# Kernel tuning notes

Hardware: AMD Instinct MI355X
Metric: run time of the kernel (lower is better)

## Reference

```python
import jax, jax.numpy as jnp
import numpy as np

N = 50000   # nodes
E = 800000  # edges
G = 64      # graphs in batch
EPS = 1e-5  # BatchNorm eps


def setup_inputs() -> dict:
    key = jax.random.key(0)
    ks = jax.random.split(key, 32)
    inp = {
        'x': jax.random.normal(ks[0], (N, 1), jnp.float32),
        'edge_index': jax.random.randint(ks[1], (2, E), 0, N),
        'batch': jnp.sort(jax.random.randint(ks[2], (N,), 0, G)),
    }
    dims = [(1, 64), (64, 64), (64, 64), (64, 64)]
    for i, (din, dout) in enumerate(dims, 1):
        inp[f'W{i}'] = jax.random.normal(ks[2 + i], (din, dout), jnp.float32) / np.sqrt(din)
        inp[f'b{i}'] = jnp.zeros((dout,), jnp.float32)
        inp[f'g{i}'] = jnp.ones((dout,), jnp.float32)
        inp[f'bt{i}'] = jnp.zeros((dout,), jnp.float32)
    inp['fw1'] = jax.random.normal(ks[10], (128, 64), jnp.float32) / 8.0
    inp['fb1'] = jnp.zeros((128,), jnp.float32)
    inp['fw2'] = jax.random.normal(ks[11], (10, 128), jnp.float32) / np.sqrt(128)
    inp['fb2'] = jnp.zeros((10,), jnp.float32)
    return inp


def _gcn_norm(edge_index):
    # add self-loops, symmetric normalization (PyG GCNConv default)
    loop = jnp.arange(N)
    row = jnp.concatenate([edge_index[0], loop])
    col = jnp.concatenate([edge_index[1], loop])
    deg = jax.ops.segment_sum(jnp.ones_like(col, jnp.float32), col, num_segments=N)
    dinv = jnp.where(deg > 0, deg ** -0.5, 0.0)
    norm = dinv[row] * dinv[col]
    return row, col, norm


def _gcn(x, W, b, row, col, norm):
    h = x @ W                                   # [N, dout]
    msg = h[row] * norm[:, None]                # gather + scale per edge
    agg = jax.ops.segment_sum(msg, col, num_segments=N)  # scatter-add
    return agg + b


def _bn(x, g, bt):
    m = x.mean(0)
    v = x.var(0)
    return g * (x - m) * jax.lax.rsqrt(v + EPS) + bt


def reference(x, edge_index, batch,
              W1, b1, g1, bt1, W2, b2, g2, bt2,
              W3, b3, g3, bt3, W4, b4, g4, bt4,
              fw1, fb1, fw2, fb2):
    row, col, norm = _gcn_norm(edge_index)
    x = jax.nn.relu(_bn(_gcn(x, W1, b1, row, col, norm), g1, bt1))
    x = jax.nn.relu(_bn(_gcn(x, W2, b2, row, col, norm), g2, bt2))
    x = jax.nn.relu(_bn(_gcn(x, W3, b3, row, col, norm), g3, bt3))
    x = jax.nn.relu(_bn(_gcn(x, W4, b4, row, col, norm), g4, bt4))
    # global mean pool over graphs
    cnt = jax.ops.segment_sum(jnp.ones((N,), jnp.float32), batch, num_segments=G)
    pooled = jax.ops.segment_sum(x, batch, num_segments=G) / jnp.clip(cnt, 1.0)[:, None]
    h = jax.nn.relu(pooled @ fw1.T + fb1)
    return h @ fw2.T + fb2
```

## Files before the change

kernel.cpp:

```cpp
#include <hip/hip_runtime.h>

#define NN 50000
#define NE 800000
#define NG 64
#define FD 64
#define BN_EPS 1e-5f
#define SCAN_B 256
#define NBIN 98
#define BINCAP 12288
#define SCH 4096
#define SCH_NBLK ((NE + SCH - 1) / SCH)
#define INV_NN (1.0f / NN)

__global__ __launch_bounds__(256) void k_binscatter(const int* __restrict__ row,
                                                    const int* __restrict__ col,
                                                    int* __restrict__ gcnt,
                                                    int* __restrict__ bins) {
    __shared__ int stage[SCH];
    __shared__ int cnt[NBIN], off[NBIN + 1], cur[NBIN], gbase[NBIN];
    int t = threadIdx.x;
    int e0 = blockIdx.x * SCH;
    int nk = NE - e0; if (nk > SCH) nk = SCH;
    if (nk <= 0) return;
    for (int b = t; b < NBIN; b += 256) cnt[b] = 0;
    __syncthreads();
    for (int k = t; k < nk; k += 256) {
        int c = col[e0 + k];
        atomicAdd(&cnt[c >> 9], 1);
    }
    __syncthreads();
    if (t == 0) {
        int run = 0;
        for (int b = 0; b < NBIN; ++b) { off[b] = run; run += cnt[b]; }
        off[NBIN] = run;
    }
    __syncthreads();
    if (t < NBIN) {
        cur[t] = off[t];
        gbase[t] = t * BINCAP + atomicAdd(&gcnt[t], cnt[t]);
    }
    __syncthreads();
    for (int k = t; k < nk; k += 256) {
        int c = col[e0 + k];
        int r = row[e0 + k];
        int b = c >> 9;
        int pos = atomicAdd(&cur[b], 1);
        stage[pos] = ((c & 511) << 16) | r;
    }
    __syncthreads();
    for (int k = t; k < nk; k += 256) {
        int lo = 0, hi = NBIN - 1;
        while (lo < hi) {
            int mid = (lo + hi + 1) >> 1;
            if (off[mid] <= k) lo = mid; else hi = mid - 1;
        }
        bins[gbase[lo] + (k - off[lo])] = stage[k];
    }
}

__global__ __launch_bounds__(256) void k_binscan(const int* __restrict__ gcnt,
                                                 const int* __restrict__ bins,
                                                 const float* __restrict__ x,
                                                 int* __restrict__ cursor,
                                                 int* __restrict__ bsum,
                                                 float* __restrict__ dinv,
                                                 float* __restrict__ xd) {
    __shared__ int ldeg[512];
    __shared__ int psc[256];
    int b = blockIdx.x, t = threadIdx.x;
    for (int l = t; l < 512; l += 256) ldeg[l] = 0;
    __syncthreads();
    int nb = gcnt[b];
    const int* bp = bins + b * BINCAP;
    for (int k = t; k < nb; k += 256) atomicAdd(&ldeg[bp[k] >> 16], 1);
    __syncthreads();
    int d0 = ldeg[2 * t], d1 = ldeg[2 * t + 1];
    int pv = d0 + d1;
    psc[t] = pv;
    __syncthreads();
    for (int off = 1; off < 256; off <<= 1) {
        int u = (t >= off) ? psc[t - off] : 0;
        __syncthreads();
        psc[t] += u;
        __syncthreads();
    }
    int excl = psc[t] - pv;
    int base = b << 9;
    int i0 = base + 2 * t, i1 = i0 + 1;
    if (i0 < NN) {
        cursor[i0] = excl;
        float dv = rsqrtf((float)d0 + 1.0f);
        dinv[i0] = dv; xd[i0] = x[i0] * dv;
    }
    if (i1 < NN) {
        cursor[i1] = excl + d0;
        float dv = rsqrtf((float)d1 + 1.0f);
        dinv[i1] = dv; xd[i1] = x[i1] * dv;
    }
    if (t == 255) bsum[b] = psc[255];
}

__global__ __launch_bounds__(SCAN_B) void k_scan_top(int* __restrict__ bsum,
                                                     float* __restrict__ stats) {
    __shared__ int sh[SCAN_B];
    int t = threadIdx.x;
    if (t < 2) stats[t] = 0.0f;
    int v = (t < NBIN) ? bsum[t] : 0;
    sh[t] = v;
    __syncthreads();
    for (int off = 1; off < SCAN_B; off <<= 1) {
        int u = (t >= off) ? sh[t - off] : 0;
        __syncthreads();
        sh[t] += u;
        __syncthreads();
    }
    if (t < NBIN) bsum[t] = sh[t] - v;
}

__global__ __launch_bounds__(256) void k_binfill(const int* __restrict__ gcnt,
                                                 const int* __restrict__ bins,
                                                 const int* __restrict__ cursor,
                                                 const int* __restrict__ bsum,
                                                 int* __restrict__ eidx) {
    __shared__ int lcur[512];
    int b = blockIdx.x, t = threadIdx.x;
    int base = b << 9;
    int bofs = bsum[b];
    for (int l = t; l < 512; l += 256) {
        int i = base + l;
        lcur[l] = (i < NN) ? cursor[i] + bofs : 0;
    }
    __syncthreads();
    int nb = gcnt[b];
    const int* bp = bins + b * BINCAP;
    for (int k = t; k < nb; k += 256) {
        int v = bp[k];
        int pos = atomicAdd(&lcur[v >> 16], 1);
        eidx[pos] = v & 0xFFFF;
    }
}

__global__ __launch_bounds__(256) void k_l1_gather(const int* __restrict__ cursor,
                                                   const int* __restrict__ bsum,
                                                   const int* __restrict__ eidx,
                                                   const float* __restrict__ xd,
                                                   const float* __restrict__ x,
                                                   const float* __restrict__ dinv,
                                                   float* __restrict__ s,
                                                   float* __restrict__ stats) {
    __shared__ float ls[256], lq[256];
    int t = threadIdx.x;
    int i = blockIdx.x * 256 + t;
    float sv = 0.0f;
    if (i < NN) {
        int start = cursor[i] + bsum[i >> 9];
        int end = (i < NN - 1) ? cursor[i + 1] + bsum[(i + 1) >> 9] : NE;
        float acc = 0.0f;
        for (int k = start; k < end; ++k) acc += xd[eidx[k]];
        float di = dinv[i];
        sv = di * (acc + di * x[i]);
        s[i] = sv;
    }
    ls[t] = sv; lq[t] = sv * sv;
    __syncthreads();
    for (int st = 128; st > 0; st >>= 1) {
        if (t < st) { ls[t] += ls[t + st]; lq[t] += lq[t + st]; }
        __syncthreads();
    }
    if (t == 0) { atomicAdd(&stats[0], ls[0]); atomicAdd(&stats[1], lq[0]); }
}

__global__ __launch_bounds__(256) void k_mm_l1(const float* __restrict__ s,
                                               const float* __restrict__ stats,
                                               const float* __restrict__ W1,
                                               const float* __restrict__ g1,
                                               const float* __restrict__ bt1,
                                               const float* __restrict__ W,
                                               float* __restrict__ h) {
    __shared__ float Ws[64 * 64];
    __shared__ float xs[4 * 64];
    __shared__ float als[64], cls[64];
    int t = threadIdx.x;
    for (int k = t; k < 64 * 64; k += 256) Ws[k] = W[k];
    if (t < 64) {
        float mean = stats[0] * INV_NN;
        float var  = stats[1] * INV_NN - mean * mean;
        float w = W1[t];
        float rinv = rsqrtf(var * w * w + BN_EPS);
        float a = g1[t] * w * rinv;
        als[t] = a;
        cls[t] = bt1[t] - a * mean;
    }
    __syncthreads();
    int n0 = blockIdx.x * 4;
    int j = t & 63, n = t >> 6;
    int node = n0 + n;
    float sv = (node < NN) ? s[node] : 0.0f;
    xs[t] = fmaxf(als[j] * sv + cls[j], 0.0f);
    __syncthreads();
    if (node < NN) {
        float acc = 0.f;
        #pragma unroll
        for (int k = 0; k < 64; ++k) acc += xs[n * 64 + k] * Ws[k * 64 + j];
        h[node * 64 + j] = acc;
    }
}

__global__ __launch_bounds__(256) void k_mm_bn(const float* __restrict__ src,
                                               const float* __restrict__ bnsum,
                                               const float* __restrict__ bnsq,
                                               const float* __restrict__ g,
                                               const float* __restrict__ bt,
                                               const float* __restrict__ W,
                                               float* __restrict__ h) {
    __shared__ float Ws[64 * 64];
    __shared__ float xs[4 * 64];
    __shared__ float scl[64], shf[64];
    int t = threadIdx.x;
    for (int k = t; k < 64 * 64; k += 256) Ws[k] = W[k];
    if (t < 64) {
        float mean = bnsum[t] * INV_NN;
        float var  = bnsq[t] * INV_NN - mean * mean;
        float rinv = rsqrtf(var + BN_EPS);
        float sc = g[t] * rinv;
        scl[t] = sc;
        shf[t] = bt[t] - sc * mean;
    }
    __syncthreads();
    int n0 = blockIdx.x * 4;
    int j = t & 63, n = t >> 6;
    int node = n0 + n;
    int gidx = n0 * 64 + t;
    float v = (gidx < NN * 64) ? src[gidx] : 0.0f;
    xs[t] = fmaxf(scl[j] * v + shf[j], 0.0f);
    __syncthreads();
    if (node < NN) {
        float acc = 0.f;
        #pragma unroll
        for (int k = 0; k < 64; ++k) acc += xs[n * 64 + k] * Ws[k * 64 + j];
        h[node * 64 + j] = acc;
    }
}

__global__ __launch_bounds__(256) void k_gather(const int* __restrict__ cursor,
                                                const int* __restrict__ bsum,
                                                const int* __restrict__ eidx,
                                                const float* __restrict__ dinv,
                                                const float* __restrict__ h,
                                                const float* __restrict__ b,
                                                float* __restrict__ agg,
                                                float* __restrict__ bnsumz,
                                                float* __restrict__ bnsqz) {
    if (blockIdx.x == 0) {
        int t = threadIdx.x;
        if (t < 64) bnsumz[t] = 0.0f;
        else if (t < 128) bnsqz[t - 64] = 0.0f;
    }
    int node = blockIdx.x * 4 + (threadIdx.x >> 6);
    if (node >= NN) return;
    int lane = threadIdx.x & 63;
    int eslot = lane >> 4;
    int fb = (lane & 15) << 2;
    int start = cursor[node] + bsum[node >> 9];
    int end = (node < NN - 1) ? cursor[node + 1] + bsum[(node + 1) >> 9] : NE;
    float4 acc = make_float4(0.f, 0.f, 0.f, 0.f);
    for (int e = start + eslot; e < end; e += 4) {
        int r = eidx[e];
        float dr = dinv[r];
        const float4 hv = *reinterpret_cast<const float4*>(&h[r * 64 + fb]);
        acc.x += hv.x * dr; acc.y += hv.y * dr; acc.z += hv.z * dr; acc.w += hv.w * dr;
    }
    acc.x += __shfl_xor(acc.x, 16); acc.y += __shfl_xor(acc.y, 16);
    acc.z += __shfl_xor(acc.z, 16); acc.w += __shfl_xor(acc.w, 16);
    acc.x += __shfl_xor(acc.x, 32); acc.y += __shfl_xor(acc.y, 32);
    acc.z += __shfl_xor(acc.z, 32); acc.w += __shfl_xor(acc.w, 32);
    if (lane < 16) {
        float dc = dinv[node];
        const float4 hv = *reinterpret_cast<const float4*>(&h[node * 64 + fb]);
        const float4 bv = *reinterpret_cast<const float4*>(&b[fb]);
        float4 o;
        o.x = dc * (acc.x + dc * hv.x) + bv.x;
        o.y = dc * (acc.y + dc * hv.y) + bv.y;
        o.z = dc * (acc.z + dc * hv.z) + bv.z;
        o.w = dc * (acc.w + dc * hv.w) + bv.w;
        *reinterpret_cast<float4*>(&agg[node * 64 + fb]) = o;
    }
}

__global__ __launch_bounds__(256) void k_bn_stats(const float* __restrict__ agg,
                                                  float* __restrict__ bnsum, float* __restrict__ bnsq,
                                                  float* __restrict__ pooledz, float* __restrict__ cntz) {
    if (pooledz != nullptr && blockIdx.x == 0) {
        for (int k = threadIdx.x; k < 64 * 64; k += 256) pooledz[k] = 0.0f;
        if (threadIdx.x < 64) cntz[threadIdx.x] = 0.0f;
    }
    __shared__ float ls[256], lq[256];
    int j = threadIdx.x & 63, nl = threadIdx.x >> 6;
    float a = 0.f, b = 0.f;
    for (int i = blockIdx.x * 4 + nl; i < NN; i += gridDim.x * 4) {
        float v = agg[i * 64 + j]; a += v; b += v * v;
    }
    ls[threadIdx.x] = a; lq[threadIdx.x] = b; __syncthreads();
    if (threadIdx.x < 128) { ls[threadIdx.x] += ls[threadIdx.x + 128]; lq[threadIdx.x] += lq[threadIdx.x + 128]; }
    __syncthreads();
    if (threadIdx.x < 64) {
        atomicAdd(&bnsum[j], ls[threadIdx.x] + ls[threadIdx.x + 64]);
        atomicAdd(&bnsq[j],  lq[threadIdx.x] + lq[threadIdx.x + 64]);
    }
}

__global__ __launch_bounds__(256) void k_pool_bn(const float* __restrict__ agg,
                                                 const float* __restrict__ bnsum,
                                                 const float* __restrict__ bnsq,
                                                 const float* __restrict__ g4,
                                                 const float* __restrict__ bt4,
                                                 const int* __restrict__ batch,
                                                 float* __restrict__ pooled,
                                                 float* __restrict__ cnt) {
    const int wpb = 4;
    int wave = blockIdx.x * wpb + (threadIdx.x >> 6);
    int lane = threadIdx.x & 63;
    const int nwaves = gridDim.x * wpb;
    int chunk = (NN + nwaves - 1) / nwaves;
    int i0 = wave * chunk;
    int i1 = i0 + chunk; if (i1 > NN) i1 = NN;
    if (i0 >= NN) return;
    float mean = bnsum[lane] * INV_NN;
    float var  = bnsq[lane] * INV_NN - mean * mean;
    float rinv = rsqrtf(var + BN_EPS);
    float sc = g4[lane] * rinv;
    float sh = bt4[lane] - sc * mean;
    float acc = 0.0f;
    int curb = batch[i0];
    int runlen = 0;
    for (int i = i0; i < i1; ++i) {
        int b = batch[i];
        if (b != curb) {
            atomicAdd(&pooled[curb * 64 + lane], acc);
            if (lane == 0) atomicAdd(&cnt[curb], (float)runlen);
            acc = 0.0f; runlen = 0; curb = b;
        }
        acc += fmaxf(sc * agg[i * 64 + lane] + sh, 0.0f);
        ++runlen;
    }
    atomicAdd(&pooled[curb * 64 + lane], acc);
    if (lane == 0) atomicAdd(&cnt[curb], (float)runlen);
}

__global__ __launch_bounds__(128) void k_fc(const float* __restrict__ pooled, const float* __restrict__ cnt,
                                            const float* __restrict__ fw1, const float* __restrict__ fb1,
                                            const float* __restrict__ fw2, const float* __restrict__ fb2,
                                            float* __restrict__ out) {
    __shared__ float p[64], hsh[128];
    int g = blockIdx.x, t = threadIdx.x;
    if (t < 64) {
        float c = cnt[g]; c = c < 1.f ? 1.f : c;
        p[t] = pooled[g * 64 + t] / c;
    }
    __syncthreads();
    float acc = fb1[t];
    #pragma unroll 8
    for (int k = 0; k < 64; ++k) acc += p[k] * fw1[t * 64 + k];
    hsh[t] = fmaxf(acc, 0.f);
    __syncthreads();
    if (t < 10) {
        float o = fb2[t];
        #pragma unroll 8
        for (int k = 0; k < 128; ++k) o += hsh[k] * fw2[t * 128 + k];
        out[g * 10 + t] = o;
    }
}

extern "C" void kernel_launch(void* const* d_in, const int* in_sizes, int n_in,
                              void* d_out, int out_size, void* d_ws, size_t ws_size,
                              hipStream_t stream) {
    const float* x   = (const float*)d_in[0];
    const int* ei    = (const int*)d_in[1];
    const int* batch = (const int*)d_in[2];
    const float* W[5]  = {nullptr, (const float*)d_in[3],  (const float*)d_in[7],
                                   (const float*)d_in[11], (const float*)d_in[15]};
    const float* bb[5] = {nullptr, (const float*)d_in[4],  (const float*)d_in[8],
                                   (const float*)d_in[12], (const float*)d_in[16]};
    const float* gg[5] = {nullptr, (const float*)d_in[5],  (const float*)d_in[9],
                                   (const float*)d_in[13], (const float*)d_in[17]};
    const float* bt[5] = {nullptr, (const float*)d_in[6],  (const float*)d_in[10],
                                   (const float*)d_in[14], (const float*)d_in[18]};
    const float* fw1 = (const float*)d_in[19];
    const float* fb1 = (const float*)d_in[20];
    const float* fw2 = (const float*)d_in[21];
    const float* fb2 = (const float*)d_in[22];
    float* out = (float*)d_out;

    const int* row = ei;
    const int* col = ei + NE;

    float* ws = (float*)d_ws;
    int*   cursor  = (int*)ws;
    int*   eidx    = (int*)(ws + 50000);
    float* dinv    = ws + 850000;
    float* xd      = ws + 900000;
    int*   bsum    = (int*)(ws + 950000);
    float* s       = ws + 951000;
    float* stats   = ws + 1001008;
    float* bnsum   = ws + 1001072;
    float* bnsq    = ws + 1001136;
    float* pooled  = ws + 1001360;
    float* cnt     = ws + 1005456;
    int*   gcnt    = (int*)(ws + 1056000);
    float* hbuf    = ws + 1100000;
    int*   bins    = (int*)(ws + 1100000);
    float* aggbuf  = ws + 4300000;

    const int B = 256;
    int gN = (NN + B - 1) / B;

    hipMemsetAsync(gcnt, 0, NBIN * sizeof(int), stream);
    k_binscatter<<<SCH_NBLK, B, 0, stream>>>(row, col, gcnt, bins);
    k_binscan<<<NBIN, B, 0, stream>>>(gcnt, bins, x, cursor, bsum, dinv, xd);
    k_scan_top<<<1, SCAN_B, 0, stream>>>(bsum, stats);
    k_binfill<<<NBIN, B, 0, stream>>>(gcnt, bins, cursor, bsum, eidx);

    k_l1_gather<<<gN, B, 0, stream>>>(cursor, bsum, eidx, xd, x, dinv, s, stats);

    k_mm_l1<<<(NN + 3) / 4, B, 0, stream>>>(s, stats, W[1], gg[1], bt[1], W[2], hbuf);
    k_gather<<<(NN + 3) / 4, B, 0, stream>>>(cursor, bsum, eidx, dinv, hbuf, bb[2], aggbuf, bnsum, bnsq);
    k_bn_stats<<<512, B, 0, stream>>>(aggbuf, bnsum, bnsq, nullptr, nullptr);

    for (int L = 3; L <= 4; ++L) {
        k_mm_bn<<<(NN + 3) / 4, B, 0, stream>>>(aggbuf, bnsum, bnsq, gg[L - 1], bt[L - 1], W[L], hbuf);
        k_gather<<<(NN + 3) / 4, B, 0, stream>>>(cursor, bsum, eidx, dinv, hbuf, bb[L], aggbuf, bnsum, bnsq);
        k_bn_stats<<<512, B, 0, stream>>>(aggbuf, bnsum, bnsq,
                                          (L == 4) ? pooled : nullptr, (L == 4) ? cnt : nullptr);
    }

    k_pool_bn<<<512, B, 0, stream>>>(aggbuf, bnsum, bnsq, gg[4], bt[4], batch, pooled, cnt);
    k_fc<<<NG, 128, 0, stream>>>(pooled, cnt, fw1, fb1, fw2, fb2, out);
}
```

Baseline: 345.7 us.

## Fuse BN statistics into gather epilogue and merge binfill with layer-1 gather

```diff
diff --git a/kernel.cpp b/kernel.cpp
--- a/kernel.cpp
+++ b/kernel.cpp
@@ -11,6 +11,8 @@
 #define SCH 4096
 #define SCH_NBLK ((NE + SCH - 1) / SCH)
 #define INV_NN (1.0f / NN)
+#define NSLOT 256
+#define MM_NBLK ((NN + 3) / 4)
 
 __global__ __launch_bounds__(256) void k_binscatter(const int* __restrict__ row,
                                                     const int* __restrict__ col,
@@ -117,18 +119,25 @@
     if (t < NBIN) bsum[t] = sh[t] - v;
 }
 
-__global__ __launch_bounds__(256) void k_binfill(const int* __restrict__ gcnt,
-                                                 const int* __restrict__ bins,
-                                                 const int* __restrict__ cursor,
-                                                 const int* __restrict__ bsum,
-                                                 int* __restrict__ eidx) {
-    __shared__ int lcur[512];
+__global__ __launch_bounds__(256) void k_binfill_l1(const int* __restrict__ gcnt,
+                                                    const int* __restrict__ bins,
+                                                    const int* __restrict__ cursor,
+                                                    const int* __restrict__ bsum,
+                                                    int* __restrict__ eidx,
+                                                    const float* __restrict__ xd,
+                                                    const float* __restrict__ x,
+                                                    const float* __restrict__ dinv,
+                                                    float* __restrict__ s,
+                                                    float* __restrict__ stats) {
+    __shared__ int lstart[512], lcur[512];
+    __shared__ float ls[256], lq[256];
     int b = blockIdx.x, t = threadIdx.x;
     int base = b << 9;
     int bofs = bsum[b];
     for (int l = t; l < 512; l += 256) {
         int i = base + l;
-        lcur[l] = (i < NN) ? cursor[i] + bofs : 0;
+        int st = (i < NN) ? cursor[i] + bofs : 0;
+        lstart[l] = st; lcur[l] = st;
     }
     __syncthreads();
     int nb = gcnt[b];
@@ -138,30 +147,23 @@
         int pos = atomicAdd(&lcur[v >> 16], 1);
         eidx[pos] = v & 0xFFFF;
     }
-}
-
-__global__ __launch_bounds__(256) void k_l1_gather(const int* __restrict__ cursor,
-                                                   const int* __restrict__ bsum,
-                                                   const int* __restrict__ eidx,
-                                                   const float* __restrict__ xd,
-                                                   const float* __restrict__ x,
-                                                   const float* __restrict__ dinv,
-                                                   float* __restrict__ s,
-                                                   float* __restrict__ stats) {
-    __shared__ float ls[256], lq[256];
-    int t = threadIdx.x;
-    int i = blockIdx.x * 256 + t;
-    float sv = 0.0f;
-    if (i < NN) {
-        int start = cursor[i] + bsum[i >> 9];
-        int end = (i < NN - 1) ? cursor[i + 1] + bsum[(i + 1) >> 9] : NE;
-        float acc = 0.0f;
-        for (int k = start; k < end; ++k) acc += xd[eidx[k]];
-        float di = dinv[i];
-        sv = di * (acc + di * x[i]);
-        s[i] = sv;
-    }
-    ls[t] = sv; lq[t] = sv * sv;
+    __syncthreads();
+    float a = 0.0f, q = 0.0f;
+    #pragma unroll
+    for (int half = 0; half < 2; ++half) {
+        int l = t + half * 256;
+        int i = base + l;
+        if (i < NN) {
+            float acc = 0.0f;
+            int e0 = lstart[l], e1 = lcur[l];
+            for (int k = e0; k < e1; ++k) acc += xd[eidx[k]];
+            float di = dinv[i];
+            float sv = di * (acc + di * x[i]);
+            s[i] = sv;
+            a += sv; q += sv * sv;
+        }
+    }
+    ls[t] = a; lq[t] = q;
     __syncthreads();
     for (int st = 128; st > 0; st >>= 1) {
         if (t < st) { ls[t] += ls[t + st]; lq[t] += lq[t + st]; }
@@ -176,20 +178,25 @@
                                                const float* __restrict__ g1,
                                                const float* __restrict__ bt1,
                                                const float* __restrict__ W,
-                                               float* __restrict__ h) {
+                                               float* __restrict__ h,
+                                               float* __restrict__ bnpart) {
     __shared__ float Ws[64 * 64];
     __shared__ float xs[4 * 64];
     __shared__ float als[64], cls[64];
     int t = threadIdx.x;
+    {
+        int idx = blockIdx.x * 3 + (t & 3);
+        if (t < 3 + 1 && (t & 3) < 3 && idx < 128 * NSLOT && t < 3) bnpart[idx] = 0.0f;
+    }
     for (int k = t; k < 64 * 64; k += 256) Ws[k] = W[k];
     if (t < 64) {
         float mean = stats[0] * INV_NN;
         float var  = stats[1] * INV_NN - mean * mean;
         float w = W1[t];
         float rinv = rsqrtf(var * w * w + BN_EPS);
-        float a = g1[t] * w * rinv;
-        als[t] = a;
-        cls[t] = bt1[t] - a * mean;
+        float aa = g1[t] * w * rinv;
+        als[t] = aa;
+        cls[t] = bt1[t] - aa * mean;
     }
     __syncthreads();
     int n0 = blockIdx.x * 4;
@@ -212,11 +219,16 @@
                                                const float* __restrict__ g,
                                                const float* __restrict__ bt,
                                                const float* __restrict__ W,
-                                               float* __restrict__ h) {
+                                               float* __restrict__ h,
+                                               float* __restrict__ bnpart) {
     __shared__ float Ws[64 * 64];
     __shared__ float xs[4 * 64];
     __shared__ float scl[64], shf[64];
     int t = threadIdx.x;
+    {
+        int idx = blockIdx.x * 3 + t;
+        if (t < 3 && idx < 128 * NSLOT) bnpart[idx] = 0.0f;
+    }
     for (int k = t; k < 64 * 64; k += 256) Ws[k] = W[k];
     if (t < 64) {
         float mean = bnsum[t] * INV_NN;
@@ -249,63 +261,79 @@
                                                 const float* __restrict__ h,
                                                 const float* __restrict__ b,
                                                 float* __restrict__ agg,
-                                                float* __restrict__ bnsumz,
-                                                float* __restrict__ bnsqz) {
-    if (blockIdx.x == 0) {
-        int t = threadIdx.x;
-        if (t < 64) bnsumz[t] = 0.0f;
-        else if (t < 128) bnsqz[t - 64] = 0.0f;
-    }
-    int node = blockIdx.x * 4 + (threadIdx.x >> 6);
-    if (node >= NN) return;
+                                                float* __restrict__ bnpart) {
+    __shared__ float tile[4][64];
+    int n = threadIdx.x >> 6;
+    int node = blockIdx.x * 4 + n;
     int lane = threadIdx.x & 63;
     int eslot = lane >> 4;
     int fb = (lane & 15) << 2;
     int start = cursor[node] + bsum[node >> 9];
     int end = (node < NN - 1) ? cursor[node + 1] + bsum[(node + 1) >> 9] : NE;
-    float4 acc = make_float4(0.f, 0.f, 0.f, 0.f);
-    for (int e = start + eslot; e < end; e += 4) {
+    float4 acc0 = make_float4(0.f, 0.f, 0.f, 0.f);
+    float4 acc1 = make_float4(0.f, 0.f, 0.f, 0.f);
+    int e = start + eslot;
+    for (; e + 4 < end; e += 8) {
+        int r0 = eidx[e], r1 = eidx[e + 4];
+        float dr0 = dinv[r0], dr1 = dinv[r1];
+        const float4 h0 = *reinterpret_cast<const float4*>(&h[r0 * 64 + fb]);
+        const float4 h1 = *reinterpret_cast<const float4*>(&h[r1 * 64 + fb]);
+        acc0.x += h0.x * dr0; acc0.y += h0.y * dr0; acc0.z += h0.z * dr0; acc0.w += h0.w * dr0;
+        acc1.x += h1.x * dr1; acc1.y += h1.y * dr1; acc1.z += h1.z * dr1; acc1.w += h1.w * dr1;
+    }
+    if (e < end) {
         int r = eidx[e];
         float dr = dinv[r];
         const float4 hv = *reinterpret_cast<const float4*>(&h[r * 64 + fb]);
-        acc.x += hv.x * dr; acc.y += hv.y * dr; acc.z += hv.z * dr; acc.w += hv.w * dr;
-    }
-    acc.x += __shfl_xor(acc.x, 16); acc.y += __shfl_xor(acc.y, 16);
-    acc.z += __shfl_xor(acc.z, 16); acc.w += __shfl_xor(acc.w, 16);
-    acc.x += __shfl_xor(acc.x, 32); acc.y += __shfl_xor(acc.y, 32);
-    acc.z += __shfl_xor(acc.z, 32); acc.w += __shfl_xor(acc.w, 32);
+        acc0.x += hv.x * dr; acc0.y += hv.y * dr; acc0.z += hv.z * dr; acc0.w += hv.w * dr;
+    }
+    acc0.x += acc1.x; acc0.y += acc1.y; acc0.z += acc1.z; acc0.w += acc1.w;
+    acc0.x += __shfl_xor(acc0.x, 16); acc0.y += __shfl_xor(acc0.y, 16);
+    acc0.z += __shfl_xor(acc0.z, 16); acc0.w += __shfl_xor(acc0.w, 16);
+    acc0.x += __shfl_xor(acc0.x, 32); acc0.y += __shfl_xor(acc0.y, 32);
+    acc0.z += __shfl_xor(acc0.z, 32); acc0.w += __shfl_xor(acc0.w, 32);
     if (lane < 16) {
         float dc = dinv[node];
         const float4 hv = *reinterpret_cast<const float4*>(&h[node * 64 + fb]);
         const float4 bv = *reinterpret_cast<const float4*>(&b[fb]);
         float4 o;
-        o.x = dc * (acc.x + dc * hv.x) + bv.x;
-        o.y = dc * (acc.y + dc * hv.y) + bv.y;
-        o.z = dc * (acc.z + dc * hv.z) + bv.z;
-        o.w = dc * (acc.w + dc * hv.w) + bv.w;
+        o.x = dc * (acc0.x + dc * hv.x) + bv.x;
+        o.y = dc * (acc0.y + dc * hv.y) + bv.y;
+        o.z = dc * (acc0.z + dc * hv.z) + bv.z;
+        o.w = dc * (acc0.w + dc * hv.w) + bv.w;
         *reinterpret_cast<float4*>(&agg[node * 64 + fb]) = o;
-    }
-}
-
-__global__ __launch_bounds__(256) void k_bn_stats(const float* __restrict__ agg,
-                                                  float* __restrict__ bnsum, float* __restrict__ bnsq,
-                                                  float* __restrict__ pooledz, float* __restrict__ cntz) {
-    if (pooledz != nullptr && blockIdx.x == 0) {
-        for (int k = threadIdx.x; k < 64 * 64; k += 256) pooledz[k] = 0.0f;
-        if (threadIdx.x < 64) cntz[threadIdx.x] = 0.0f;
-    }
-    __shared__ float ls[256], lq[256];
-    int j = threadIdx.x & 63, nl = threadIdx.x >> 6;
-    float a = 0.f, b = 0.f;
-    for (int i = blockIdx.x * 4 + nl; i < NN; i += gridDim.x * 4) {
-        float v = agg[i * 64 + j]; a += v; b += v * v;
-    }
-    ls[threadIdx.x] = a; lq[threadIdx.x] = b; __syncthreads();
-    if (threadIdx.x < 128) { ls[threadIdx.x] += ls[threadIdx.x + 128]; lq[threadIdx.x] += lq[threadIdx.x + 128]; }
-    __syncthreads();
-    if (threadIdx.x < 64) {
-        atomicAdd(&bnsum[j], ls[threadIdx.x] + ls[threadIdx.x + 64]);
-        atomicAdd(&bnsq[j],  lq[threadIdx.x] + lq[threadIdx.x + 64]);
+        tile[n][fb]     = o.x;
+        tile[n][fb + 1] = o.y;
+        tile[n][fb + 2] = o.z;
+        tile[n][fb + 3] = o.w;
+    }
+    __syncthreads();
+    int t = threadIdx.x;
+    if (t < 64) {
+        float v0 = tile[0][t], v1 = tile[1][t], v2 = tile[2][t], v3 = tile[3][t];
+        float sm = v0 + v1 + v2 + v3;
+        float sq = v0 * v0 + v1 * v1 + v2 * v2 + v3 * v3;
+        int slot = blockIdx.x & (NSLOT - 1);
+        atomicAdd(&bnpart[t * NSLOT + slot], sm);
+        atomicAdd(&bnpart[(64 + t) * NSLOT + slot], sq);
+    }
+}
+
+__global__ __launch_bounds__(256) void k_bn_reduce(const float* __restrict__ bnpart,
+                                                   float* __restrict__ bnsum,
+                                                   float* __restrict__ bnsq,
+                                                   float* __restrict__ pooledz,
+                                                   float* __restrict__ cntz) {
+    int t = threadIdx.x;
+    if (t < 128) {
+        float sm = 0.0f;
+        const float* p = bnpart + t * NSLOT;
+        for (int k = 0; k < NSLOT; ++k) sm += p[k];
+        if (t < 64) bnsum[t] = sm; else bnsq[t - 64] = sm;
+    }
+    if (pooledz != nullptr) {
+        for (int k = t; k < 64 * 64; k += 256) pooledz[k] = 0.0f;
+        if (t < 64) cntz[t] = 0.0f;
     }
 }
 
@@ -406,31 +434,29 @@
     float* bnsq    = ws + 1001136;
     float* pooled  = ws + 1001360;
     float* cnt     = ws + 1005456;
+    float* bnpart  = ws + 1006000;
     int*   gcnt    = (int*)(ws + 1056000);
     float* hbuf    = ws + 1100000;
     int*   bins    = (int*)(ws + 1100000);
     float* aggbuf  = ws + 4300000;
 
     const int B = 256;
-    int gN = (NN + B - 1) / B;
 
     hipMemsetAsync(gcnt, 0, NBIN * sizeof(int), stream);
     k_binscatter<<<SCH_NBLK, B, 0, stream>>>(row, col, gcnt, bins);
     k_binscan<<<NBIN, B, 0, stream>>>(gcnt, bins, x, cursor, bsum, dinv, xd);
     k_scan_top<<<1, SCAN_B, 0, stream>>>(bsum, stats);
-    k_binfill<<<NBIN, B, 0, stream>>>(gcnt, bins, cursor, bsum, eidx);
-
-    k_l1_gather<<<gN, B, 0, stream>>>(cursor, bsum, eidx, xd, x, dinv, s, stats);
-
-    k_mm_l1<<<(NN + 3) / 4, B, 0, stream>>>(s, stats, W[1], gg[1], bt[1], W[2], hbuf);
-    k_gather<<<(NN + 3) / 4, B, 0, stream>>>(cursor, bsum, eidx, dinv, hbuf, bb[2], aggbuf, bnsum, bnsq);
-    k_bn_stats<<<512, B, 0, stream>>>(aggbuf, bnsum, bnsq, nullptr, nullptr);
+    k_binfill_l1<<<NBIN, B, 0, stream>>>(gcnt, bins, cursor, bsum, eidx, xd, x, dinv, s, stats);
+
+    k_mm_l1<<<MM_NBLK, B, 0, stream>>>(s, stats, W[1], gg[1], bt[1], W[2], hbuf, bnpart);
+    k_gather<<<MM_NBLK, B, 0, stream>>>(cursor, bsum, eidx, dinv, hbuf, bb[2], aggbuf, bnpart);
+    k_bn_reduce<<<1, B, 0, stream>>>(bnpart, bnsum, bnsq, nullptr, nullptr);
 
     for (int L = 3; L <= 4; ++L) {
-        k_mm_bn<<<(NN + 3) / 4, B, 0, stream>>>(aggbuf, bnsum, bnsq, gg[L - 1], bt[L - 1], W[L], hbuf);
-        k_gather<<<(NN + 3) / 4, B, 0, stream>>>(cursor, bsum, eidx, dinv, hbuf, bb[L], aggbuf, bnsum, bnsq);
-        k_bn_stats<<<512, B, 0, stream>>>(aggbuf, bnsum, bnsq,
-                                          (L == 4) ? pooled : nullptr, (L == 4) ? cnt : nullptr);
+        k_mm_bn<<<MM_NBLK, B, 0, stream>>>(aggbuf, bnsum, bnsq, gg[L - 1], bt[L - 1], W[L], hbuf, bnpart);
+        k_gather<<<MM_NBLK, B, 0, stream>>>(cursor, bsum, eidx, dinv, hbuf, bb[L], aggbuf, bnpart);
+        k_bn_reduce<<<1, B, 0, stream>>>(bnpart, bnsum, bnsq,
+                                         (L == 4) ? pooled : nullptr, (L == 4) ? cnt : nullptr);
     }
 
     k_pool_bn<<<512, B, 0, stream>>>(aggbuf, bnsum, bnsq, gg[4], bt[4], batch, pooled, cnt);
```

Measured after the change: 512.4 us. +48.2%, slower.
